# Kernel optimization log

Measured on AMD Instinct MI355X. Metric: run time of the kernel, lower is better.

Reference implementation:

```python
import jax, jax.numpy as jnp
import numpy as np

BN_EPS = 1e-5
DIST_EPS = 1e-8


def setup_inputs() -> dict:
    key = jax.random.key(0)
    ks = jax.random.split(key, 8)
    B, N, S = 8, 8192, 2048
    D_unk, D_kn = 128, 256
    inp = {
        "unknown_xyz": jax.random.uniform(ks[0], (B, N, 3), dtype=jnp.float32),
        "known_xyz": jax.random.uniform(ks[1], (B, S, 3), dtype=jnp.float32),
        "unknown_points": jax.random.normal(ks[2], (B, N, D_unk), dtype=jnp.float32),
        "known_points": jax.random.normal(ks[3], (B, S, D_kn), dtype=jnp.float32),
        "W0": jax.random.normal(ks[4], (256, 384), dtype=jnp.float32) * (1.0 / np.sqrt(384)),
        "b0": jnp.zeros((256,), jnp.float32),
        "g0": jnp.ones((256,), jnp.float32),
        "beta0": jnp.zeros((256,), jnp.float32),
        "W1": jax.random.normal(ks[5], (128, 256), dtype=jnp.float32) * (1.0 / np.sqrt(256)),
        "b1": jnp.zeros((128,), jnp.float32),
        "g1": jnp.ones((128,), jnp.float32),
        "beta1": jnp.zeros((128,), jnp.float32),
    }
    return inp


def _three_nn(unknown_xyz, known_xyz):
    # squared pairwise distances [B, N, S]
    d = jnp.sum((unknown_xyz[:, :, None, :] - known_xyz[:, None, :, :]) ** 2, axis=-1)
    neg_top, idx = jax.lax.top_k(-d, 3)  # 3 smallest distances
    return -neg_top, idx  # dists [B,N,3], idx [B,N,3]


def _conv_bn_relu(x, W, b, g, beta):
    # x: [B, N, Cin]; 1x1 Conv1d == per-point linear
    y = jnp.einsum("bnc,oc->bno", x, W) + b
    mean = jnp.mean(y, axis=(0, 1))
    var = jnp.var(y, axis=(0, 1))  # biased, as BatchNorm training forward
    y = g * (y - mean) * jax.lax.rsqrt(var + BN_EPS) + beta
    return jax.nn.relu(y)


def reference(unknown_xyz, known_xyz, unknown_points, known_points,
              W0, b0, g0, beta0, W1, b1, g1, beta1):
    dists, idx = _three_nn(unknown_xyz, known_xyz)
    dist_recip = 1.0 / (dists + DIST_EPS)
    weight = dist_recip / jnp.sum(dist_recip, axis=2, keepdims=True)  # [B,N,3]
    # gather 3 neighbor features: [B,N,3,D_kn]
    gathered = jax.vmap(lambda f, i: f[i])(known_points, idx)
    interpolated = jnp.sum(weight[..., None] * gathered, axis=2)  # [B,N,D_kn]
    x = jnp.concatenate([unknown_points, interpolated], axis=-1)  # [B,N,384]
    x = _conv_bn_relu(x, W0, b0, g0, beta0)
    x = _conv_bn_relu(x, W1, b1, g1, beta1)
    return x  # [B, N, 128]
```

## Files before the change

kernel.cpp:

```cpp
#include <hip/hip_runtime.h>
#include <hip/hip_bf16.h>


typedef __attribute__((ext_vector_type(8))) short short8;
typedef __attribute__((ext_vector_type(4))) float f32x4;

#define BB 8
#define NN 8192
#define SS 2048
#define M_TOT (BB * NN)
#define K1DIM 384
#define N1DIM 256
#define K2DIM 256
#define N2DIM 128
#define NCH 8
#define CHS (SS / NCH)
#define BK 64

__device__ __forceinline__ unsigned short f2bf(float f) {
    unsigned int x = __float_as_uint(f);
    unsigned int r = x + 0x7fffu + ((x >> 16) & 1u);
    return (unsigned short)(r >> 16);
}
__device__ __forceinline__ float bf2f(unsigned short u) {
    return __uint_as_float(((unsigned int)u) << 16);
}

__device__ __forceinline__ void gload_lds16(const void* g, void* lds) {
    __builtin_amdgcn_global_load_lds(
        (const __attribute__((address_space(1))) unsigned int*)g,
        (__attribute__((address_space(3))) unsigned int*)lds, 16, 0, 0);
}

__global__ __launch_bounds__(256) void nn_cand_kernel(
    const float* __restrict__ uxyz,
    const float* __restrict__ kxyz,
    float2* __restrict__ cand)
{
    __shared__ float kx[CHS], ky[CHS], kz[CHS];

    const int tid  = threadIdx.x;
    const int bid  = blockIdx.x;
    const int ch   = bid & 7;
    const int tile = (bid >> 3) & 31;
    const int b    = bid >> 8;

    const float* kb = kxyz + ((size_t)b * SS + ch * CHS) * 3;
    kx[tid] = kb[tid * 3 + 0];
    ky[tid] = kb[tid * 3 + 1];
    kz[tid] = kb[tid * 3 + 2];
    __syncthreads();

    const int n = tile * 256 + tid;
    const float* up = uxyz + ((size_t)b * NN + n) * 3;
    const float ux = up[0], uy = up[1], uz = up[2];

    float d0 = 1e30f, d1 = 1e30f, d2 = 1e30f;
    int   i0 = 0, i1 = 0, i2 = 0;
#pragma unroll 8
    for (int s = 0; s < CHS; ++s) {
        float dx = ux - kx[s], dy = uy - ky[s], dz = uz - kz[s];
        float d = fmaf(dx, dx, fmaf(dy, dy, dz * dz));
        bool lt2 = d < d2, lt1 = d < d1, lt0 = d < d0;
        d2 = lt1 ? d1 : (lt2 ? d : d2);
        i2 = lt1 ? i1 : (lt2 ? s : i2);
        d1 = lt0 ? d0 : (lt1 ? d : d1);
        i1 = lt0 ? i0 : (lt1 ? s : i1);
        d0 = lt0 ? d  : d0;
        i0 = lt0 ? s  : i0;
    }
    const int base = ch * CHS;
    float2* c = cand + ((size_t)ch * M_TOT + (size_t)b * NN + n) * 3;
    c[0] = make_float2(d0, __int_as_float(base + i0));
    c[1] = make_float2(d1, __int_as_float(base + i1));
    c[2] = make_float2(d2, __int_as_float(base + i2));
}

__global__ __launch_bounds__(256) void merge_interp_kernel(
    const float2* __restrict__ cand,
    const float* __restrict__ upts,
    const float* __restrict__ kpts,
    unsigned short* __restrict__ x)
{
    __shared__ int   sidx[64][3];
    __shared__ float sw[64][3];

    const int tid = threadIdx.x;
    const int bid = blockIdx.x;
    const int b   = bid & 7;
    const int pn  = (bid >> 3) * 64;

    if (tid < 64) {
        const size_t pt = (size_t)b * NN + pn + tid;
        float d0 = 1e30f, d1 = 1e30f, d2 = 1e30f;
        int   i0 = 0, i1 = 0, i2 = 0;
#pragma unroll
        for (int ch = 0; ch < NCH; ++ch) {
            const float2* c = cand + ((size_t)ch * M_TOT + pt) * 3;
#pragma unroll
            for (int j = 0; j < 3; ++j) {
                float d = c[j].x;
                int   i = __float_as_int(c[j].y);
                bool lt2 = d < d2, lt1 = d < d1, lt0 = d < d0;
                d2 = lt1 ? d1 : (lt2 ? d : d2);
                i2 = lt1 ? i1 : (lt2 ? i : i2);
                d1 = lt0 ? d0 : (lt1 ? d : d1);
                i1 = lt0 ? i0 : (lt1 ? i : i1);
                d0 = lt0 ? d  : d0;
                i0 = lt0 ? i  : i0;
            }
        }
        float r0 = 1.0f / (d0 + 1e-8f);
        float r1 = 1.0f / (d1 + 1e-8f);
        float r2 = 1.0f / (d2 + 1e-8f);
        float rs = 1.0f / (r0 + r1 + r2);
        sidx[tid][0] = i0; sidx[tid][1] = i1; sidx[tid][2] = i2;
        sw[tid][0] = r0 * rs; sw[tid][1] = r1 * rs; sw[tid][2] = r2 * rs;
    }
    __syncthreads();

    const int wv = tid >> 6, lane = tid & 63;
    const float* kpb = kpts + (size_t)b * SS * N1DIM;
    const float* upb = upts + (size_t)b * NN * 128;
    for (int p = wv; p < 64; p += 4) {
        const int j0 = sidx[p][0], j1 = sidx[p][1], j2 = sidx[p][2];
        const float w0 = sw[p][0], w1 = sw[p][1], w2 = sw[p][2];
        unsigned short* xr = x + ((size_t)b * NN + pn + p) * K1DIM;

        float4 f0 = *(const float4*)(kpb + (size_t)j0 * 256 + lane * 4);
        float4 f1 = *(const float4*)(kpb + (size_t)j1 * 256 + lane * 4);
        float4 f2 = *(const float4*)(kpb + (size_t)j2 * 256 + lane * 4);
        ushort4 o;
        o.x = f2bf(w0 * f0.x + w1 * f1.x + w2 * f2.x);
        o.y = f2bf(w0 * f0.y + w1 * f1.y + w2 * f2.y);
        o.z = f2bf(w0 * f0.z + w1 * f1.z + w2 * f2.z);
        o.w = f2bf(w0 * f0.w + w1 * f1.w + w2 * f2.w);
        *(ushort4*)(xr + 128 + lane * 4) = o;

        if (lane < 32) {
            float4 u = *(const float4*)(upb + ((size_t)(pn + p)) * 128 + lane * 4);
            ushort4 q;
            q.x = f2bf(u.x); q.y = f2bf(u.y); q.z = f2bf(u.z); q.w = f2bf(u.w);
            *(ushort4*)(xr + lane * 4) = q;
        }
    }
}

__global__ __launch_bounds__(256) void cvt_w_kernel(
    const float* __restrict__ W0, const float* __restrict__ W1,
    unsigned short* __restrict__ Wb0, unsigned short* __restrict__ Wb1)
{
    int i = blockIdx.x * 256 + threadIdx.x;
    if (i < N1DIM * K1DIM) Wb0[i] = f2bf(W0[i]);
    if (i < N2DIM * K2DIM) Wb1[i] = f2bf(W1[i]);
}

#define G1_NT (K1DIM / BK)
__global__ __launch_bounds__(512, 2) void gemm1_kernel(
    const unsigned short* __restrict__ X,
    const unsigned short* __restrict__ Wb,
    unsigned short* __restrict__ Y,
    float* __restrict__ stats)
{
    __shared__ __align__(128) unsigned char smem[2 * 49152];

    const int tid = threadIdx.x;
    const int l = tid & 63, w = tid >> 6;
    const int wm = w >> 2, wn = w & 3;
    const int row0 = blockIdx.x * 128;
    const int srow = l >> 3;
    const int sbo  = (l & 7) * 16;

    f32x4 acc[4][4];
#pragma unroll
    for (int m = 0; m < 4; ++m)
#pragma unroll
        for (int n = 0; n < 4; ++n) {
            f32x4 z = {0.f, 0.f, 0.f, 0.f};
            acc[m][n] = z;
        }

    const unsigned char* Xb = (const unsigned char*)X;
    const unsigned char* Bb = (const unsigned char*)Wb;

    auto stage = [&](int buf, int t) {
        unsigned char* Al = smem + buf * 49152;
        unsigned char* Bl = Al + 16384;
        const int k0b = t * (BK * 2);
#pragma unroll
        for (int i = 0; i < 2; ++i) {
            const int r = w * 16 + i * 8 + srow;
            gload_lds16(Xb + (size_t)(row0 + r) * (K1DIM * 2) + k0b + (sbo ^ ((r & 7) << 4)),
                        Al + r * 128 + sbo);
        }
#pragma unroll
        for (int i = 0; i < 4; ++i) {
            const int r = w * 32 + i * 8 + srow;
            gload_lds16(Bb + (size_t)r * (K1DIM * 2) + k0b + (sbo ^ ((r & 7) << 4)),
                        Bl + r * 128 + sbo);
        }
    };

    auto compute = [&](int buf) {
        const unsigned char* Al = smem + buf * 49152;
        const unsigned char* Bl = Al + 16384;
#pragma unroll
        for (int ks = 0; ks < 2; ++ks) {
            const int bo = ks * 64 + (l >> 4) * 16;
            short8 a[4], bq[4];
#pragma unroll
            for (int m = 0; m < 4; ++m) {
                const int r = wm * 64 + m * 16 + (l & 15);
                a[m] = *(const short8*)(Al + r * 128 + (bo ^ ((r & 7) << 4)));
            }
#pragma unroll
            for (int n = 0; n < 4; ++n) {
                const int r = wn * 64 + n * 16 + (l & 15);
                bq[n] = *(const short8*)(Bl + r * 128 + (bo ^ ((r & 7) << 4)));
            }
#pragma unroll
            for (int m = 0; m < 4; ++m)
#pragma unroll
                for (int n = 0; n < 4; ++n)
                    acc[m][n] = __builtin_amdgcn_mfma_f32_16x16x32_bf16(
                        a[m], bq[n], acc[m][n], 0, 0, 0);
        }
    };

    stage(0, 0);
    __syncthreads();
#pragma unroll
    for (int t = 0; t < G1_NT; ++t) {
        const int cur = t & 1;
        if (t + 1 < G1_NT) stage(cur ^ 1, t + 1);
        compute(cur);
        __syncthreads();
    }

    float s1[4] = {0.f, 0.f, 0.f, 0.f}, s2[4] = {0.f, 0.f, 0.f, 0.f};
#pragma unroll
    for (int m = 0; m < 4; ++m) {
        const int row = row0 + wm * 64 + m * 16 + (l >> 4) * 4;
#pragma unroll
        for (int n = 0; n < 4; ++n) {
            const int col = wn * 64 + n * 16 + (l & 15);
            f32x4 v = acc[m][n];
#pragma unroll
            for (int r = 0; r < 4; ++r) {
                float f = v[r];
                Y[(size_t)(row + r) * N1DIM + col] = f2bf(f);
                s1[n] += f;
                s2[n] += f * f;
            }
        }
    }
#pragma unroll
    for (int n = 0; n < 4; ++n) {
        s1[n] += __shfl_xor(s1[n], 16, 64);
        s1[n] += __shfl_xor(s1[n], 32, 64);
        s2[n] += __shfl_xor(s2[n], 16, 64);
        s2[n] += __shfl_xor(s2[n], 32, 64);
    }
    if (l < 16) {
#pragma unroll
        for (int n = 0; n < 4; ++n) {
            const int col = wn * 64 + n * 16 + l;
            atomicAdd(&stats[col], s1[n]);
            atomicAdd(&stats[N1DIM + col], s2[n]);
        }
    }
}

#define G2_NT (K2DIM / BK)
__global__ __launch_bounds__(512, 4) void gemm2_kernel(
    const unsigned short* __restrict__ Y0,
    const unsigned short* __restrict__ Wb,
    const float* __restrict__ gm,
    const float* __restrict__ ga,
    float* __restrict__ Y1,
    float* __restrict__ stats)
{
    __shared__ __align__(128) unsigned char smem[2 * 32768];
    __shared__ float sgm[K2DIM], sga[K2DIM];

    const int tid = threadIdx.x;
    const int l = tid & 63, w = tid >> 6;
    const int wm = w >> 2, wn = w & 3;
    const int row0 = blockIdx.x * 128;
    const int srow = l >> 3;
    const int sbo  = (l & 7) * 16;
    const int lr  = tid >> 2;
    const int lcq = tid & 3;

    f32x4 acc[4][2];
#pragma unroll
    for (int m = 0; m < 4; ++m)
#pragma unroll
        for (int n = 0; n < 2; ++n) {
            f32x4 z = {0.f, 0.f, 0.f, 0.f};
            acc[m][n] = z;
        }

    const unsigned char* Bb = (const unsigned char*)Wb;
    short8 areg0, areg1;

    auto issueA = [&](int t) {
        const unsigned short* src = Y0 + (size_t)(row0 + lr) * K2DIM + t * BK + lcq * 16;
        areg0 = *(const short8*)src;
        areg1 = *(const short8*)(src + 8);
    };
    auto stageB = [&](int buf, int t) {
        unsigned char* Bl = smem + buf * 32768 + 16384;
        const int k0b = t * (BK * 2);
#pragma unroll
        for (int i = 0; i < 2; ++i) {
            const int r = w * 16 + i * 8 + srow;
            gload_lds16(Bb + (size_t)r * (K2DIM * 2) + k0b + (sbo ^ ((r & 7) << 4)),
                        Bl + r * 128 + sbo);
        }
    };
    auto xformA = [&](int buf, int t) {
        unsigned char* Al = smem + buf * 32768;
        const int kb = t * BK + lcq * 16;
        short8 o0, o1;
#pragma unroll
        for (int j = 0; j < 8; ++j) {
            float f = bf2f((unsigned short)areg0[j]);
            f = fmaxf(fmaf(f, sgm[kb + j], sga[kb + j]), 0.f);
            o0[j] = (short)f2bf(f);
            float g = bf2f((unsigned short)areg1[j]);
            g = fmaxf(fmaf(g, sgm[kb + 8 + j], sga[kb + 8 + j]), 0.f);
            o1[j] = (short)f2bf(g);
        }
        const int bo = lcq * 32;
        *(short8*)(Al + lr * 128 + ((bo) ^ ((lr & 7) << 4))) = o0;
        *(short8*)(Al + lr * 128 + ((bo + 16) ^ ((lr & 7) << 4))) = o1;
    };
    auto compute = [&](int buf) {
        const unsigned char* Al = smem + buf * 32768;
        const unsigned char* Bl = Al + 16384;
#pragma unroll
        for (int ks = 0; ks < 2; ++ks) {
            const int bo = ks * 64 + (l >> 4) * 16;
            short8 a[4], bq[2];
#pragma unroll
            for (int m = 0; m < 4; ++m) {
                const int r = wm * 64 + m * 16 + (l & 15);
                a[m] = *(const short8*)(Al + r * 128 + (bo ^ ((r & 7) << 4)));
            }
#pragma unroll
            for (int n = 0; n < 2; ++n) {
                const int r = wn * 32 + n * 16 + (l & 15);
                bq[n] = *(const short8*)(Bl + r * 128 + (bo ^ ((r & 7) << 4)));
            }
#pragma unroll
            for (int m = 0; m < 4; ++m)
#pragma unroll
                for (int n = 0; n < 2; ++n)
                    acc[m][n] = __builtin_amdgcn_mfma_f32_16x16x32_bf16(
                        a[m], bq[n], acc[m][n], 0, 0, 0);
        }
    };

    if (tid < K2DIM) { sgm[tid] = gm[tid]; sga[tid] = ga[tid]; }
    issueA(0);
    stageB(0, 0);
    __syncthreads();
    xformA(0, 0);
    __syncthreads();

#pragma unroll
    for (int t = 0; t < G2_NT; ++t) {
        const int cur = t & 1;
        if (t + 1 < G2_NT) { issueA(t + 1); stageB(cur ^ 1, t + 1); }
        compute(cur);
        if (t + 1 < G2_NT) xformA(cur ^ 1, t + 1);
        __syncthreads();
    }

    float s1[2] = {0.f, 0.f}, s2[2] = {0.f, 0.f};
#pragma unroll
    for (int m = 0; m < 4; ++m) {
        const int row = row0 + wm * 64 + m * 16 + (l >> 4) * 4;
#pragma unroll
        for (int n = 0; n < 2; ++n) {
            const int col = wn * 32 + n * 16 + (l & 15);
            f32x4 v = acc[m][n];
#pragma unroll
            for (int r = 0; r < 4; ++r) {
                float f = v[r];
                Y1[(size_t)(row + r) * N2DIM + col] = f;
                s1[n] += f;
                s2[n] += f * f;
            }
        }
    }
#pragma unroll
    for (int n = 0; n < 2; ++n) {
        s1[n] += __shfl_xor(s1[n], 16, 64);
        s1[n] += __shfl_xor(s1[n], 32, 64);
        s2[n] += __shfl_xor(s2[n], 16, 64);
        s2[n] += __shfl_xor(s2[n], 32, 64);
    }
    if (l < 16) {
#pragma unroll
        for (int n = 0; n < 2; ++n) {
            const int col = wn * 32 + n * 16 + l;
            atomicAdd(&stats[col], s1[n]);
            atomicAdd(&stats[N2DIM + col], s2[n]);
        }
    }
}

__global__ void finalize_stats_kernel(
    const float* __restrict__ stats, const float* __restrict__ g,
    const float* __restrict__ beta, float* __restrict__ gm,
    float* __restrict__ ga, int C)
{
    int c = blockIdx.x * blockDim.x + threadIdx.x;
    if (c < C) {
        const float inv = 1.0f / (float)M_TOT;
        float mean = stats[c] * inv;
        float var = stats[C + c] * inv - mean * mean;
        float m = g[c] * rsqrtf(var + 1e-5f);
        gm[c] = m;
        ga[c] = beta[c] - mean * m;
    }
}

__global__ __launch_bounds__(256) void bn_out_kernel(
    const float* __restrict__ Y1, const float* __restrict__ gm,
    const float* __restrict__ ga, float* __restrict__ out)
{
    const int total = M_TOT * N2DIM / 4;
    for (int i = blockIdx.x * 256 + threadIdx.x; i < total; i += gridDim.x * 256) {
        float4 v = ((const float4*)Y1)[i];
        const int cg = (i & 31) * 4;
        float4 m = *(const float4*)(gm + cg);
        float4 a = *(const float4*)(ga + cg);
        float4 o;
        o.x = fmaxf(fmaf(v.x, m.x, a.x), 0.f);
        o.y = fmaxf(fmaf(v.y, m.y, a.y), 0.f);
        o.z = fmaxf(fmaf(v.z, m.z, a.z), 0.f);
        o.w = fmaxf(fmaf(v.w, m.w, a.w), 0.f);
        ((float4*)out)[i] = o;
    }
}

extern "C" void kernel_launch(void* const* d_in, const int* in_sizes, int n_in,
                              void* d_out, int out_size, void* d_ws, size_t ws_size,
                              hipStream_t stream)
{
    const float* uxyz  = (const float*)d_in[0];
    const float* kxyz  = (const float*)d_in[1];
    const float* upts  = (const float*)d_in[2];
    const float* kpts  = (const float*)d_in[3];
    const float* W0    = (const float*)d_in[4];
    const float* g0    = (const float*)d_in[6];
    const float* beta0 = (const float*)d_in[7];
    const float* W1    = (const float*)d_in[8];
    const float* g1    = (const float*)d_in[10];
    const float* beta1 = (const float*)d_in[11];
    float* out = (float*)d_out;

    char* ws = (char*)d_ws;
    const size_t off_x   = 0;
    const size_t off_y0  = 50331648;
    const size_t off_w0  = off_y0 + 33554432;
    const size_t off_w1  = off_w0 + 196608;
    const size_t off_f   = off_w1 + 65536;

    unsigned short* x    = (unsigned short*)(ws + off_x);
    float*          y1   = (float*)(ws + off_x);
    unsigned short* y0   = (unsigned short*)(ws + off_y0);
    float2*         cand = (float2*)(ws + off_y0);
    unsigned short* wb0  = (unsigned short*)(ws + off_w0);
    unsigned short* wb1  = (unsigned short*)(ws + off_w1);
    float* F = (float*)(ws + off_f);
    float* stats0 = F;
    float* stats1 = F + 512;
    float* gm0 = F + 768;
    float* ga0 = F + 1024;
    float* gm1 = F + 1280;
    float* ga1 = F + 1408;

    hipMemsetAsync(stats0, 0, 768 * sizeof(float), stream);

    cvt_w_kernel<<<384, 256, 0, stream>>>(W0, W1, wb0, wb1);
    nn_cand_kernel<<<2048, 256, 0, stream>>>(uxyz, kxyz, cand);
    merge_interp_kernel<<<1024, 256, 0, stream>>>(cand, upts, kpts, x);
    gemm1_kernel<<<M_TOT / 128, 512, 0, stream>>>(x, wb0, y0, stats0);
    finalize_stats_kernel<<<1, 256, 0, stream>>>(stats0, g0, beta0, gm0, ga0, N1DIM);
    gemm2_kernel<<<M_TOT / 128, 512, 0, stream>>>(y0, wb1, gm0, ga0, y1, stats1);
    finalize_stats_kernel<<<1, 256, 0, stream>>>(stats1, g1, beta1, gm1, ga1, N2DIM);
    bn_out_kernel<<<2048, 256, 0, stream>>>(y1, gm1, ga1, out);
}
```

Measured before the change: 176.2 us.

## Pack distance and index into sortable uint keys for min/max top-3 selection

The nearest-neighbour scan now packs each truncated distance with its 11-bit index into one 32-bit key, so the top-3 insertion becomes a chain of integer min/max ops instead of compare-and-select on separate distance and index registers. Known xyz is packed into float4 for uniform broadcast loads, replacing the LDS staging and barrier. The merge stage keeps six candidates from the truncated keys, recomputes exact distances and sorts 64-bit keys to recover the exact top-3. Candidate storage is halved to a plane-major uint layout, at the cost of the extra exact re-check in the merge and a tie-break that may differ from top_k.

```diff
diff --git a/kernel.cpp b/kernel.cpp
--- a/kernel.cpp
+++ b/kernel.cpp
@@ -17,6 +17,9 @@
 #define CHS (SS / NCH)
 #define BK 64
 
+#define KEY_MASK 0xFFFFF800u
+#define IDX_MASK 0x7FFu
+
 __device__ __forceinline__ unsigned short f2bf(float f) {
     unsigned int x = __float_as_uint(f);
     unsigned int r = x + 0x7fffu + ((x >> 16) & 1u);
@@ -34,50 +37,48 @@
 
 __global__ __launch_bounds__(256) void nn_cand_kernel(
     const float* __restrict__ uxyz,
-    const float* __restrict__ kxyz,
-    float2* __restrict__ cand)
-{
-    __shared__ float kx[CHS], ky[CHS], kz[CHS];
-
+    const float4* __restrict__ kpack,
+    unsigned int* __restrict__ cand)
+{
     const int tid  = threadIdx.x;
     const int bid  = blockIdx.x;
     const int ch   = bid & 7;
     const int tile = (bid >> 3) & 31;
     const int b    = bid >> 8;
 
-    const float* kb = kxyz + ((size_t)b * SS + ch * CHS) * 3;
-    kx[tid] = kb[tid * 3 + 0];
-    ky[tid] = kb[tid * 3 + 1];
-    kz[tid] = kb[tid * 3 + 2];
-    __syncthreads();
-
     const int n = tile * 256 + tid;
     const float* up = uxyz + ((size_t)b * NN + n) * 3;
     const float ux = up[0], uy = up[1], uz = up[2];
 
-    float d0 = 1e30f, d1 = 1e30f, d2 = 1e30f;
-    int   i0 = 0, i1 = 0, i2 = 0;
+    const float4* kb = kpack + (size_t)b * SS + ch * CHS;
+    const int base = ch * CHS;
+
+    unsigned int k0 = 0xFFFFFFFFu, k1 = 0xFFFFFFFFu, k2 = 0xFFFFFFFFu;
 #pragma unroll 8
     for (int s = 0; s < CHS; ++s) {
-        float dx = ux - kx[s], dy = uy - ky[s], dz = uz - kz[s];
+        float4 kc = kb[s];
+        float dx = kc.x - ux, dy = kc.y - uy, dz = kc.z - uz;
         float d = fmaf(dx, dx, fmaf(dy, dy, dz * dz));
-        bool lt2 = d < d2, lt1 = d < d1, lt0 = d < d0;
-        d2 = lt1 ? d1 : (lt2 ? d : d2);
-        i2 = lt1 ? i1 : (lt2 ? s : i2);
-        d1 = lt0 ? d0 : (lt1 ? d : d1);
-        i1 = lt0 ? i0 : (lt1 ? s : i1);
-        d0 = lt0 ? d  : d0;
-        i0 = lt0 ? s  : i0;
-    }
-    const int base = ch * CHS;
-    float2* c = cand + ((size_t)ch * M_TOT + (size_t)b * NN + n) * 3;
-    c[0] = make_float2(d0, __int_as_float(base + i0));
-    c[1] = make_float2(d1, __int_as_float(base + i1));
-    c[2] = make_float2(d2, __int_as_float(base + i2));
+        unsigned int key = (__float_as_uint(d) & KEY_MASK) | (unsigned int)(base + s);
+        unsigned int a0 = min(key, k0);
+        unsigned int m  = max(key, k0);
+        k0 = a0;
+        unsigned int a1 = min(m, k1);
+        m = max(m, k1);
+        k1 = a1;
+        k2 = min(m, k2);
+    }
+
+    const size_t pt = (size_t)b * NN + n;
+    cand[(size_t)(ch * 3 + 0) * M_TOT + pt] = k0;
+    cand[(size_t)(ch * 3 + 1) * M_TOT + pt] = k1;
+    cand[(size_t)(ch * 3 + 2) * M_TOT + pt] = k2;
 }
 
 __global__ __launch_bounds__(256) void merge_interp_kernel(
-    const float2* __restrict__ cand,
+    const unsigned int* __restrict__ cand,
+    const float4* __restrict__ kpack,
+    const float* __restrict__ uxyz,
     const float* __restrict__ upts,
     const float* __restrict__ kpts,
     unsigned short* __restrict__ x)
@@ -92,29 +93,52 @@
 
     if (tid < 64) {
         const size_t pt = (size_t)b * NN + pn + tid;
-        float d0 = 1e30f, d1 = 1e30f, d2 = 1e30f;
-        int   i0 = 0, i1 = 0, i2 = 0;
+
+        unsigned int k[6];
+#pragma unroll
+        for (int i = 0; i < 6; ++i) k[i] = 0xFFFFFFFFu;
 #pragma unroll
         for (int ch = 0; ch < NCH; ++ch) {
-            const float2* c = cand + ((size_t)ch * M_TOT + pt) * 3;
 #pragma unroll
             for (int j = 0; j < 3; ++j) {
-                float d = c[j].x;
-                int   i = __float_as_int(c[j].y);
-                bool lt2 = d < d2, lt1 = d < d1, lt0 = d < d0;
-                d2 = lt1 ? d1 : (lt2 ? d : d2);
-                i2 = lt1 ? i1 : (lt2 ? i : i2);
-                d1 = lt0 ? d0 : (lt1 ? d : d1);
-                i1 = lt0 ? i0 : (lt1 ? i : i1);
-                d0 = lt0 ? d  : d0;
-                i0 = lt0 ? i  : i0;
-            }
-        }
+                unsigned int t = cand[(size_t)(ch * 3 + j) * M_TOT + pt];
+#pragma unroll
+                for (int i = 0; i < 6; ++i) {
+                    unsigned int a = min(k[i], t);
+                    t = max(k[i], t);
+                    k[i] = a;
+                }
+            }
+        }
+
+        const float* up = uxyz + pt * 3;
+        const float ux = up[0], uy = up[1], uz = up[2];
+        const float4* kpb4 = kpack + (size_t)b * SS;
+        unsigned long long e[6];
+#pragma unroll
+        for (int i = 0; i < 6; ++i) {
+            unsigned int idx = k[i] & IDX_MASK;
+            float4 kc = kpb4[idx];
+            float dx = kc.x - ux, dy = kc.y - uy, dz = kc.z - uz;
+            float d = fmaf(dx, dx, fmaf(dy, dy, dz * dz));
+            e[i] = ((unsigned long long)__float_as_uint(d) << 32) | idx;
+        }
+#pragma unroll
+        for (int i = 0; i < 3; ++i)
+#pragma unroll
+            for (int j = i + 1; j < 6; ++j)
+                if (e[j] < e[i]) { unsigned long long t = e[i]; e[i] = e[j]; e[j] = t; }
+
+        float d0 = __uint_as_float((unsigned int)(e[0] >> 32));
+        float d1 = __uint_as_float((unsigned int)(e[1] >> 32));
+        float d2 = __uint_as_float((unsigned int)(e[2] >> 32));
         float r0 = 1.0f / (d0 + 1e-8f);
         float r1 = 1.0f / (d1 + 1e-8f);
         float r2 = 1.0f / (d2 + 1e-8f);
         float rs = 1.0f / (r0 + r1 + r2);
-        sidx[tid][0] = i0; sidx[tid][1] = i1; sidx[tid][2] = i2;
+        sidx[tid][0] = (int)(e[0] & IDX_MASK);
+        sidx[tid][1] = (int)(e[1] & IDX_MASK);
+        sidx[tid][2] = (int)(e[2] & IDX_MASK);
         sw[tid][0] = r0 * rs; sw[tid][1] = r1 * rs; sw[tid][2] = r2 * rs;
     }
     __syncthreads();
@@ -148,11 +172,17 @@
 
 __global__ __launch_bounds__(256) void cvt_w_kernel(
     const float* __restrict__ W0, const float* __restrict__ W1,
-    unsigned short* __restrict__ Wb0, unsigned short* __restrict__ Wb1)
+    const float* __restrict__ kxyz,
+    unsigned short* __restrict__ Wb0, unsigned short* __restrict__ Wb1,
+    float4* __restrict__ kpack)
 {
     int i = blockIdx.x * 256 + threadIdx.x;
     if (i < N1DIM * K1DIM) Wb0[i] = f2bf(W0[i]);
     if (i < N2DIM * K2DIM) Wb1[i] = f2bf(W1[i]);
+    if (i < BB * SS) {
+        const float* p = kxyz + (size_t)i * 3;
+        kpack[i] = make_float4(p[0], p[1], p[2], 0.0f);
+    }
 }
 
 #define G1_NT (K1DIM / BK)
@@ -473,7 +503,8 @@
     unsigned short* x    = (unsigned short*)(ws + off_x);
     float*          y1   = (float*)(ws + off_x);
     unsigned short* y0   = (unsigned short*)(ws + off_y0);
-    float2*         cand = (float2*)(ws + off_y0);
+    unsigned int*   cand = (unsigned int*)(ws + off_y0);
+    float4*         kpack = (float4*)(ws + off_y0 + 8388608);
     unsigned short* wb0  = (unsigned short*)(ws + off_w0);
     unsigned short* wb1  = (unsigned short*)(ws + off_w1);
     float* F = (float*)(ws + off_f);
@@ -486,9 +517,9 @@
 
     hipMemsetAsync(stats0, 0, 768 * sizeof(float), stream);
 
-    cvt_w_kernel<<<384, 256, 0, stream>>>(W0, W1, wb0, wb1);
-    nn_cand_kernel<<<2048, 256, 0, stream>>>(uxyz, kxyz, cand);
-    merge_interp_kernel<<<1024, 256, 0, stream>>>(cand, upts, kpts, x);
+    cvt_w_kernel<<<384, 256, 0, stream>>>(W0, W1, kxyz, wb0, wb1, kpack);
+    nn_cand_kernel<<<2048, 256, 0, stream>>>(uxyz, kpack, cand);
+    merge_interp_kernel<<<1024, 256, 0, stream>>>(cand, kpack, uxyz, upts, kpts, x);
     gemm1_kernel<<<M_TOT / 128, 512, 0, stream>>>(x, wb0, y0, stats0);
     finalize_stats_kernel<<<1, 256, 0, stream>>>(stats0, g0, beta0, gm0, ga0, N1DIM);
     gemm2_kernel<<<M_TOT / 128, 512, 0, stream>>>(y0, wb1, gm0, ga0, y1, stats1);
```

After: 163.0 us. -7.5%, faster.
